# Kernel tuning notes

Hardware: AMD Instinct MI355X
Metric: run time of the kernel (lower is better)

Reference implementation:

```python
import jax, jax.numpy as jnp
import numpy as np

B, N, D = 16, 1000, 256
K_MAX = 512  # static upper bound on union size (k1 + k2 < K_MAX)


def setup_inputs() -> dict:
    key = jax.random.key(0)
    ks = jax.random.split(key, 6)
    a = jax.random.uniform(ks[0], (B, N, N), jnp.float32)
    a = a + jnp.swapaxes(a, 1, 2)  # symmetric
    adj = (a > 1.8).astype(jnp.float32)  # sparse-ish symmetric adjacency
    H1 = jax.random.normal(ks[1], (B, N, D), jnp.float32)
    H2 = jax.random.normal(ks[2], (B, N, D), jnp.float32)
    # per-batch permutations of node ids: row j of H_i corresponds to node idx_i[b, j]
    idx1 = jax.vmap(lambda k: jax.random.permutation(k, N))(jax.random.split(ks[3], B)).astype(jnp.int32)
    idx2 = jax.vmap(lambda k: jax.random.permutation(k, N))(jax.random.split(ks[4], B)).astype(jnp.int32)
    k1 = jax.random.randint(ks[5], (B,), 1, K_MAX // 2, jnp.int32)
    k2 = jax.random.randint(jax.random.fold_in(key, 7), (B,), 1, K_MAX // 2, jnp.int32)
    return {"adj": adj, "H1": H1, "H2": H2, "idx1": idx1, "idx2": idx2, "k1": k1, "k2": k2}


def _pool_one(adj_b, H1_b, H2_b, i1, i2, kk1, kk2):
    # adj_b: [N,N], H1_b/H2_b: [N,D], i1/i2: [N] node-id permutations, kk1/kk2: scalar keep counts
    pos = jnp.arange(N)
    # membership masks over node ids: node i1[j] selected iff j < kk1
    m1 = jnp.zeros((N,), bool).at[i1].set(pos < kk1)
    m2 = jnp.zeros((N,), bool).at[i2].set(pos < kk2)
    union = m1 | m2
    inter = m1 & m2
    # inverse permutations: position of node v within index list i1/i2
    inv1 = jnp.zeros((N,), jnp.int32).at[i1].set(pos.astype(jnp.int32))
    inv2 = jnp.zeros((N,), jnp.int32).at[i2].set(pos.astype(jnp.int32))
    H1n = H1_b[inv1]  # [N,D] features re-indexed by node id
    H2n = H2_b[inv2]
    # merged per-node feature: average on intersection, single-branch otherwise
    h = jnp.where(inter[:, None], 0.5 * (H1n + H2n),
                  jnp.where(m1[:, None], H1n,
                            jnp.where(m2[:, None], H2n, jnp.zeros_like(H1n))))
    # stable sort: union nodes first (ascending node id), then the rest; take K_MAX slots
    order = jnp.argsort(jnp.logical_not(union))[:K_MAX]
    valid = union[order]  # contiguous prefix of True
    new_mask = valid.astype(adj_b.dtype)  # [K_MAX]
    S = adj_b[order] * new_mask[:, None]  # [K_MAX, N] selected adjacency rows
    new_H = h[order] * new_mask[:, None]  # [K_MAX, D]
    new_adj = S @ adj_b @ S.T  # [K_MAX, K_MAX]
    return new_H, new_adj, new_mask


def reference(adj, H1, H2, idx1, idx2, k1, k2):
    return jax.vmap(_pool_one)(adj, H1, H2, idx1, idx2, k1, k2)
```

## Files before the change

### kernel.cpp

```cpp
#include <hip/hip_runtime.h>

#define BATCH 16
#define NN 1000
#define DD 256
#define KMAX 512

#define META_STRIDE 2560
#define AP 1024

typedef unsigned char u8;
typedef __attribute__((ext_vector_type(4))) int i32x4;

#define LD4(p) (*(const float4*)(p))

__device__ __forceinline__ void meta_body(
    int b, int t,
    const int* __restrict__ idx1, const int* __restrict__ idx2,
    const int* __restrict__ k1, const int* __restrict__ k2,
    int* __restrict__ meta) {
  __shared__ int sc[256];
  __shared__ int sU;
  int* inv1 = meta + (size_t)b * META_STRIDE;
  int* inv2 = inv1 + NN;
  int* order = inv2 + NN;
  int* Uptr = order + KMAX;
  const int* i1 = idx1 + (size_t)b * NN;
  const int* i2 = idx2 + (size_t)b * NN;
  for (int j = t; j < NN; j += 256) {
    inv1[i1[j]] = j;
    inv2[i2[j]] = j;
  }
  __syncthreads();
  int kk1 = k1[b], kk2 = k2[b];
  int base = t * 4;
  int un[4];
  int cnt = 0;
  for (int i = 0; i < 4; ++i) {
    int v = base + i;
    int u = 0;
    if (v < NN) u = (inv1[v] < kk1) || (inv2[v] < kk2);
    un[i] = u;
    cnt += u;
  }
  sc[t] = cnt;
  __syncthreads();
  for (int off = 1; off < 256; off <<= 1) {
    int v = (t >= off) ? sc[t - off] : 0;
    __syncthreads();
    sc[t] += v;
    __syncthreads();
  }
  int pref = sc[t] - cnt;
  for (int i = 0; i < 4; ++i)
    if (un[i]) order[pref++] = base + i;
  if (t == 255) {
    sU = sc[255];
    *Uptr = sc[255];
  }
  __syncthreads();
  int U = sU;
  for (int r = U + t; r < KMAX; r += 256) order[r] = 0;
}

__global__ __launch_bounds__(256) void meta_kernel(
    const int* __restrict__ idx1, const int* __restrict__ idx2,
    const int* __restrict__ k1, const int* __restrict__ k2,
    int* __restrict__ meta) {
  meta_body(blockIdx.x, threadIdx.x, idx1, idx2, k1, k2, meta);
}

__device__ __forceinline__ unsigned int pack4u8(float4 f) {
  return (unsigned int)(u8)f.x | ((unsigned int)(u8)f.y << 8) |
         ((unsigned int)(u8)f.z << 16) | ((unsigned int)(u8)f.w << 24);
}

__global__ __launch_bounds__(256) void convmeta_kernel(
    const float* __restrict__ adj, u8* __restrict__ adjb,
    const int* __restrict__ idx1, const int* __restrict__ idx2,
    const int* __restrict__ k1, const int* __restrict__ k2,
    int* __restrict__ meta) {
  int g = blockIdx.x;
  int tid = threadIdx.x;
  if (g >= 4096) {
    meta_body(g - 4096, tid, idx1, idx2, k1, k2, meta);
    return;
  }
  int xcd = g & 7, slot = g >> 3;
  int b = xcd + 8 * (slot >> 8);
  int r = (slot & 255) * 4 + (tid >> 6);
  int lane = tid & 63;
  int c0 = lane * 16;
  unsigned int w0 = 0, w1 = 0, w2 = 0, w3 = 0;
  if (r < NN) {
    const float* src = adj + ((size_t)b * NN + r) * NN + c0;
    int nv = NN - c0;
    if (nv >= 16) {
      w0 = pack4u8(LD4(src));
      w1 = pack4u8(LD4(src + 4));
      w2 = pack4u8(LD4(src + 8));
      w3 = pack4u8(LD4(src + 12));
    } else if (nv >= 8) {
      w0 = pack4u8(LD4(src));
      w1 = pack4u8(LD4(src + 4));
    }
  }
  *(int4*)(adjb + ((size_t)b * AP + r) * AP + c0) = make_int4(w0, w1, w2, w3);
}

__global__ __launch_bounds__(256) void conv_fb_kernel(
    const float* __restrict__ adj, u8* __restrict__ adjb, int bbase) {
  int bz = blockIdx.y;
  int b = bbase + bz;
  int tid = threadIdx.x;
  int r = blockIdx.x * 4 + (tid >> 6);
  int lane = tid & 63;
  int c0 = lane * 16;
  unsigned int w0 = 0, w1 = 0, w2 = 0, w3 = 0;
  if (r < NN) {
    const float* src = adj + ((size_t)b * NN + r) * NN + c0;
    int nv = NN - c0;
    if (nv >= 16) {
      w0 = pack4u8(LD4(src));
      w1 = pack4u8(LD4(src + 4));
      w2 = pack4u8(LD4(src + 8));
      w3 = pack4u8(LD4(src + 12));
    } else if (nv >= 8) {
      w0 = pack4u8(LD4(src));
      w1 = pack4u8(LD4(src + 4));
    }
  }
  *(int4*)(adjb + ((size_t)bz * AP + r) * AP + c0) = make_int4(w0, w1, w2, w3);
}

__device__ __forceinline__ void feat_row(
    const float* __restrict__ H1, const float* __restrict__ H2,
    const int* __restrict__ k1, const int* __restrict__ k2,
    const int* __restrict__ meta, float* __restrict__ outH,
    float* __restrict__ outMask, int b, int r, int l) {
  const int* inv1 = meta + (size_t)b * META_STRIDE;
  const int* inv2 = inv1 + NN;
  const int* order = inv2 + NN;
  int U = order[KMAX];
  float4* oH = (float4*)(outH + ((size_t)b * KMAX + r) * DD) + l;
  if (r >= U) {
    *oH = make_float4(0.f, 0.f, 0.f, 0.f);
    if (l == 0) outMask[(size_t)b * KMAX + r] = 0.f;
    return;
  }
  int v = order[r];
  int j1 = inv1[v];
  int j2 = inv2[v];
  bool in1 = j1 < k1[b];
  bool in2 = j2 < k2[b];
  const float4* h1 = (const float4*)(H1 + ((size_t)b * NN + j1) * DD) + l;
  const float4* h2 = (const float4*)(H2 + ((size_t)b * NN + j2) * DD) + l;
  float4 o;
  if (in1 && in2) {
    float4 a = *h1, c = *h2;
    o = make_float4(0.5f * (a.x + c.x), 0.5f * (a.y + c.y),
                    0.5f * (a.z + c.z), 0.5f * (a.w + c.w));
  } else if (in1) {
    o = *h1;
  } else {
    o = *h2;
  }
  *oH = o;
  if (l == 0) outMask[(size_t)b * KMAX + r] = 1.f;
}

__global__ __launch_bounds__(256) void feat_kernel(
    const float* __restrict__ H1, const float* __restrict__ H2,
    const int* __restrict__ k1, const int* __restrict__ k2,
    const int* __restrict__ meta,
    float* __restrict__ outH, float* __restrict__ outMask, int bbase) {
  int tid = threadIdx.x;
  int r = blockIdx.x * 4 + (tid >> 6);
  int b = blockIdx.y + bbase;
  feat_row(H1, H2, k1, k2, meta, outH, outMask, b, r, tid & 63);
}

template<int WHICH, int BM, int BN, bool PIN, bool FEAT>
__global__ __launch_bounds__(256) void mm_kernel(
    const u8* __restrict__ adjb, u8* __restrict__ Tb,
    const int* __restrict__ meta, float* __restrict__ outAdj,
    const float* __restrict__ H1, const float* __restrict__ H2,
    const int* __restrict__ k1, const int* __restrict__ k2,
    float* __restrict__ outH, float* __restrict__ outMask, int bbase) {
  constexpr int MR = BM / 32;
  constexpr int NR = BN / 32;
  constexpr int LA = (BM * 128) / 4096;
  constexpr int LB = (BN * 128) / 4096;
  constexpr int LL = LA + LB;
  constexpr int CT_TILES = (WHICH == 1 ? AP : KMAX) / BN;
  constexpr int RT_TILES = KMAX / BM;
  constexpr int TILES = RT_TILES * CT_TILES;
  constexpr int MMBLK = 8 * 2 * TILES;
  constexpr int NKT = AP / 128;

  int tid = threadIdx.x;

  if (FEAT && PIN && (int)blockIdx.x >= MMBLK) {
    int g2 = blockIdx.x - MMBLK;
    int xcd = g2 & 7;
    int slot = g2 >> 3;
    int b = xcd + 8 * (slot >> 6);
    int rb = slot & 63;
    int l = tid & 63;
#pragma unroll
    for (int pass = 0; pass < 2; ++pass) {
      int r = rb * 8 + pass * 4 + (tid >> 6);
      feat_row(H1, H2, k1, k2, meta, outH, outMask, b, r, l);
    }
    return;
  }

  int bz, rt, ct;
  if (PIN) {
    int g = blockIdx.x;
    int xcd = g & 7;
    int slot = g >> 3;
    bz = xcd + 8 * (slot / TILES);
    int tt = slot % TILES;
    rt = tt / CT_TILES;
    ct = tt % CT_TILES;
  } else {
    bz = blockIdx.z;
    rt = blockIdx.y;
    ct = blockIdx.x;
  }
  int b = PIN ? bz : (bz + bbase);

  const int* order = meta + (size_t)b * META_STRIDE + 2 * NN;
  int U = order[KMAX];
  int lane = tid & 63;
  int w = tid >> 6;
  int wr = w >> 1, wc = w & 1;

  __shared__ __align__(16) u8 A0[BM * 128];
  __shared__ __align__(16) u8 B0[BN * 128];
  __shared__ __align__(16) u8 A1[BM * 128];
  __shared__ __align__(16) u8 B1[BN * 128];
  __shared__ int sOrd[64];

  const u8* adjbB = adjb + (size_t)bz * AP * AP;
  const u8* TbB = Tb + (size_t)bz * KMAX * AP;

  bool active;
  if (WHICH == 1) {
    active = (rt * BM < U);
    if (!active) return;
  } else {
    active = (rt * BM < U) && (ct * BN < U);
  }

  if (tid < 64) sOrd[tid] = order[((WHICH == 1) ? rt * BM : ct * BN) + tid];
  __syncthreads();

  i32x4 acc[MR][NR] = {};

#define WAITV(N) asm volatile("s_waitcnt vmcnt(%0)" :: "i"(N) : "memory")
#define BARx() do { asm volatile("" ::: "memory"); __builtin_amdgcn_s_barrier(); \
                    asm volatile("" ::: "memory"); } while (0)

#define STAGE(ABUF, BBUF, KT)                                                  \
  {                                                                            \
    int k0 = (KT) * 128;                                                       \
    _Pragma("unroll")                                                          \
    for (int i = 0; i < LA; ++i) {                                             \
      int p = i * 256 + tid;                                                   \
      int r = p >> 3, cp = p & 7;                                              \
      int cs = cp ^ (r & 7);                                                   \
      const u8* src = (WHICH == 1)                                             \
          ? adjbB + (size_t)sOrd[r] * AP + k0 + cs * 16                        \
          : TbB + (size_t)(rt * BM + r) * AP + k0 + cs * 16;                   \
      u8* dst = (ABUF) + (size_t)(i * 256 + (tid & 192)) * 16;                 \
      __builtin_amdgcn_global_load_lds(                                        \
          (const __attribute__((address_space(1))) void*)src,                  \
          (__attribute__((address_space(3))) void*)dst, 16, 0, 0);             \
    }                                                                          \
    _Pragma("unroll")                                                          \
    for (int i = 0; i < LB; ++i) {                                             \
      int p = i * 256 + tid;                                                   \
      int r = p >> 3, cp = p & 7;                                              \
      int cs = cp ^ (r & 7);                                                   \
      const u8* src = (WHICH == 1)                                             \
          ? adjbB + (size_t)(ct * BN + r) * AP + k0 + cs * 16                  \
          : adjbB + (size_t)sOrd[r] * AP + k0 + cs * 16;                       \
      u8* dst = (BBUF) + (size_t)(i * 256 + (tid & 192)) * 16;                 \
      __builtin_amdgcn_global_load_lds(                                        \
          (const __attribute__((address_space(1))) void*)src,                  \
          (__attribute__((address_space(3))) void*)dst, 16, 0, 0);             \
    }                                                                          \
  }

#define COMPUTE128(ABUF, BBUF)                                                 \
  {                                                                            \
    _Pragma("unroll")                                                          \
    for (int s = 0; s < 2; ++s) {                                              \
      i32x4 a[MR], bv[NR];                                                     \
      _Pragma("unroll")                                                        \
      for (int m = 0; m < MR; ++m) {                                           \
        int row = wr * (MR * 16) + m * 16 + (lane & 15);                       \
        int c = (s * 4 + (lane >> 4)) ^ (row & 7);                             \
        a[m] = *(const i32x4*)((ABUF) + row * 128 + c * 16);                   \
      }                                                                        \
      _Pragma("unroll")                                                        \
      for (int n = 0; n < NR; ++n) {                                           \
        int row = wc * (NR * 16) + n * 16 + (lane & 15);                       \
        int c = (s * 4 + (lane >> 4)) ^ (row & 7);                             \
        bv[n] = *(const i32x4*)((BBUF) + row * 128 + c * 16);                  \
      }                                                                        \
      __builtin_amdgcn_s_setprio(1);                                           \
      _Pragma("unroll")                                                        \
      for (int m = 0; m < MR; ++m)                                             \
        _Pragma("unroll")                                                      \
        for (int n = 0; n < NR; ++n)                                           \
          acc[m][n] = __builtin_amdgcn_mfma_i32_16x16x64_i8(a[m], bv[n],       \
                                                            acc[m][n], 0, 0, 0); \
      __builtin_amdgcn_s_setprio(0);                                           \
    }                                                                          \
  }

  if (active) {
    STAGE(A0, B0, 0);
    STAGE(A1, B1, 1);
#pragma unroll 1
    for (int t = 0; t < NKT - 2; t += 2) {
      WAITV(LL);
      BARx();
      COMPUTE128(A0, B0);
      BARx();
      STAGE(A0, B0, t + 2);
      WAITV(LL);
      BARx();
      COMPUTE128(A1, B1);
      BARx();
      STAGE(A1, B1, t + 3);
    }
    WAITV(LL);
    BARx();
    COMPUTE128(A0, B0);
    WAITV(0);
    BARx();
    COMPUTE128(A1, B1);
  }
#undef STAGE
#undef COMPUTE128
#undef WAITV
#undef BARx

  if (WHICH == 1) {
    u8* TbW = Tb + (size_t)bz * KMAX * AP;
#pragma unroll
    for (int m = 0; m < MR; ++m)
#pragma unroll
      for (int n = 0; n < NR; ++n)
#pragma unroll
        for (int i = 0; i < 4; ++i) {
          int row = rt * BM + wr * (MR * 16) + m * 16 + ((lane >> 4) << 2) + i;
          int col = ct * BN + wc * (NR * 16) + n * 16 + (lane & 15);
          TbW[(size_t)row * AP + col] = (u8)acc[m][n][i];
        }
  } else {
    float* O = outAdj + (size_t)b * KMAX * KMAX;
#pragma unroll
    for (int m = 0; m < MR; ++m)
#pragma unroll
      for (int n = 0; n < NR; ++n)
#pragma unroll
        for (int i = 0; i < 4; ++i) {
          int row = rt * BM + wr * (MR * 16) + m * 16 + ((lane >> 4) << 2) + i;
          int col = ct * BN + wc * (NR * 16) + n * 16 + (lane & 15);
          float v = (row < U && col < U) ? (float)acc[m][n][i] : 0.f;
          O[(size_t)row * KMAX + col] = v;
        }
  }
}

extern "C" void kernel_launch(void* const* d_in, const int* in_sizes, int n_in,
                              void* d_out, int out_size, void* d_ws, size_t ws_size,
                              hipStream_t stream) {
  const float* adj = (const float*)d_in[0];
  const float* H1 = (const float*)d_in[1];
  const float* H2 = (const float*)d_in[2];
  const int* idx1 = (const int*)d_in[3];
  const int* idx2 = (const int*)d_in[4];
  const int* k1 = (const int*)d_in[5];
  const int* k2 = (const int*)d_in[6];

  float* outH = (float*)d_out;
  float* outAdj = outH + (size_t)BATCH * KMAX * DD;
  float* outMask = outAdj + (size_t)BATCH * KMAX * KMAX;

  int* meta = (int*)d_ws;
  size_t meta_bytes = (size_t)BATCH * META_STRIDE * sizeof(int);
  size_t meta_al = (meta_bytes + 255) & ~(size_t)255;

  size_t adjb_one = (size_t)AP * AP;
  size_t T_one = (size_t)KMAX * AP;
  size_t per_b = adjb_one + T_one;

  int chunk = 1;
  if (ws_size > meta_al + per_b)
    chunk = (int)((ws_size - meta_al) / per_b);
  if (chunk > BATCH) chunk = BATCH;
  if (chunk < 1) chunk = 1;

  u8* adjb = (u8*)((char*)d_ws + meta_al);
  u8* Tb = adjb + (size_t)chunk * adjb_one;

  if (chunk == BATCH) {
    convmeta_kernel<<<dim3(4096 + 16), 256, 0, stream>>>(adj, adjb, idx1, idx2,
                                                         k1, k2, meta);
    mm_kernel<1, 64, 128, true, true><<<dim3(2048), 256, 0, stream>>>(
        adjb, Tb, meta, outAdj, H1, H2, k1, k2, outH, outMask, 0);
    mm_kernel<2, 64, 64, true, false><<<dim3(1024), 256, 0, stream>>>(
        adjb, Tb, meta, outAdj, H1, H2, k1, k2, outH, outMask, 0);
  } else {
    meta_kernel<<<dim3(BATCH), 256, 0, stream>>>(idx1, idx2, k1, k2, meta);
    feat_kernel<<<dim3(KMAX / 4, BATCH), 256, 0, stream>>>(H1, H2, k1, k2, meta,
                                                           outH, outMask, 0);
    for (int bb = 0; bb < BATCH; bb += chunk) {
      int nb = (BATCH - bb < chunk) ? (BATCH - bb) : chunk;
      conv_fb_kernel<<<dim3(256, nb), 256, 0, stream>>>(adj, adjb, bb);
      mm_kernel<1, 64, 128, false, false><<<dim3(8, 8, nb), 256, 0, stream>>>(
          adjb, Tb, meta, outAdj, H1, H2, k1, k2, outH, outMask, bb);
      mm_kernel<2, 64, 64, false, false><<<dim3(8, 8, nb), 256, 0, stream>>>(
          adjb, Tb, meta, outAdj, H1, H2, k1, k2, outH, outMask, bb);
    }
  }
}
```

Measured before the change: 39.79 us.

## Use 4-stage LDS pipeline with 64x64 tiles and coalesced u8 conversion

Replaces the double-buffered A/B LDS staging with a four-buffer ring that prefetches three k-tiles ahead and needs one barrier per step instead of two. The first GEMM is fixed to 64x64 tiles, so it launches more blocks (3072 grid) and gets more parallelism per batch. The fp32-to-u8 adjacency conversion now has each lane handle strided 4-element chunks, giving coalesced 4-byte stores instead of 16-byte per-lane chunks. Extra LDS use and smaller tiles may reduce occupancy or data reuse.

```diff
diff --git a/kernel.cpp b/kernel.cpp
--- a/kernel.cpp
+++ b/kernel.cpp
@@ -74,6 +74,20 @@
          ((unsigned int)(u8)f.z << 16) | ((unsigned int)(u8)f.w << 24);
 }
 
+__device__ __forceinline__ void conv_rows(
+    const float* __restrict__ adj, u8* __restrict__ adjb,
+    int b_src, int b_dst, int r, int l) {
+  const float* srcrow = adj + ((size_t)b_src * NN + r) * NN;
+  u8* dstrow = adjb + ((size_t)b_dst * AP + r) * AP;
+#pragma unroll
+  for (int j = 0; j < 4; ++j) {
+    int idx = l + 64 * j;
+    unsigned int w = 0;
+    if (r < NN && idx < 250) w = pack4u8(LD4(srcrow + idx * 4));
+    *(unsigned int*)(dstrow + idx * 4) = w;
+  }
+}
+
 __global__ __launch_bounds__(256) void convmeta_kernel(
     const float* __restrict__ adj, u8* __restrict__ adjb,
     const int* __restrict__ idx1, const int* __restrict__ idx2,
@@ -88,48 +102,15 @@
   int xcd = g & 7, slot = g >> 3;
   int b = xcd + 8 * (slot >> 8);
   int r = (slot & 255) * 4 + (tid >> 6);
-  int lane = tid & 63;
-  int c0 = lane * 16;
-  unsigned int w0 = 0, w1 = 0, w2 = 0, w3 = 0;
-  if (r < NN) {
-    const float* src = adj + ((size_t)b * NN + r) * NN + c0;
-    int nv = NN - c0;
-    if (nv >= 16) {
-      w0 = pack4u8(LD4(src));
-      w1 = pack4u8(LD4(src + 4));
-      w2 = pack4u8(LD4(src + 8));
-      w3 = pack4u8(LD4(src + 12));
-    } else if (nv >= 8) {
-      w0 = pack4u8(LD4(src));
-      w1 = pack4u8(LD4(src + 4));
-    }
-  }
-  *(int4*)(adjb + ((size_t)b * AP + r) * AP + c0) = make_int4(w0, w1, w2, w3);
+  conv_rows(adj, adjb, b, b, r, tid & 63);
 }
 
 __global__ __launch_bounds__(256) void conv_fb_kernel(
     const float* __restrict__ adj, u8* __restrict__ adjb, int bbase) {
   int bz = blockIdx.y;
-  int b = bbase + bz;
   int tid = threadIdx.x;
   int r = blockIdx.x * 4 + (tid >> 6);
-  int lane = tid & 63;
-  int c0 = lane * 16;
-  unsigned int w0 = 0, w1 = 0, w2 = 0, w3 = 0;
-  if (r < NN) {
-    const float* src = adj + ((size_t)b * NN + r) * NN + c0;
-    int nv = NN - c0;
-    if (nv >= 16) {
-      w0 = pack4u8(LD4(src));
-      w1 = pack4u8(LD4(src + 4));
-      w2 = pack4u8(LD4(src + 8));
-      w3 = pack4u8(LD4(src + 12));
-    } else if (nv >= 8) {
-      w0 = pack4u8(LD4(src));
-      w1 = pack4u8(LD4(src + 4));
-    }
-  }
-  *(int4*)(adjb + ((size_t)bz * AP + r) * AP + c0) = make_int4(w0, w1, w2, w3);
+  conv_rows(adj, adjb, bbase + bz, bz, r, tid & 63);
 }
 
 __device__ __forceinline__ void feat_row(
@@ -179,23 +160,20 @@
   feat_row(H1, H2, k1, k2, meta, outH, outMask, b, r, tid & 63);
 }
 
-template<int WHICH, int BM, int BN, bool PIN, bool FEAT>
+template<int WHICH, bool PIN, bool FEAT>
 __global__ __launch_bounds__(256) void mm_kernel(
     const u8* __restrict__ adjb, u8* __restrict__ Tb,
     const int* __restrict__ meta, float* __restrict__ outAdj,
     const float* __restrict__ H1, const float* __restrict__ H2,
     const int* __restrict__ k1, const int* __restrict__ k2,
     float* __restrict__ outH, float* __restrict__ outMask, int bbase) {
-  constexpr int MR = BM / 32;
-  constexpr int NR = BN / 32;
-  constexpr int LA = (BM * 128) / 4096;
-  constexpr int LB = (BN * 128) / 4096;
-  constexpr int LL = LA + LB;
+  constexpr int BM = 64, BN = 64;
+  constexpr int MR = 2, NR = 2;
+  constexpr int LA = 2, LB = 2;
   constexpr int CT_TILES = (WHICH == 1 ? AP : KMAX) / BN;
   constexpr int RT_TILES = KMAX / BM;
   constexpr int TILES = RT_TILES * CT_TILES;
   constexpr int MMBLK = 8 * 2 * TILES;
-  constexpr int NKT = AP / 128;
 
   int tid = threadIdx.x;
 
@@ -236,10 +214,8 @@
   int w = tid >> 6;
   int wr = w >> 1, wc = w & 1;
 
-  __shared__ __align__(16) u8 A0[BM * 128];
-  __shared__ __align__(16) u8 B0[BN * 128];
-  __shared__ __align__(16) u8 A1[BM * 128];
-  __shared__ __align__(16) u8 B1[BN * 128];
+  __shared__ __align__(16) u8 As[4][BM * 128];
+  __shared__ __align__(16) u8 Bs[4][BN * 128];
   __shared__ int sOrd[64];
 
   const u8* adjbB = adjb + (size_t)bz * AP * AP;
@@ -262,8 +238,10 @@
 #define BARx() do { asm volatile("" ::: "memory"); __builtin_amdgcn_s_barrier(); \
                     asm volatile("" ::: "memory"); } while (0)
 
-#define STAGE(ABUF, BBUF, KT)                                                  \
+#define STAGE(BI, KT)                                                          \
   {                                                                            \
+    u8* sa_ = &As[(BI)][0];                                                    \
+    u8* sb_ = &Bs[(BI)][0];                                                    \
     int k0 = (KT) * 128;                                                       \
     _Pragma("unroll")                                                          \
     for (int i = 0; i < LA; ++i) {                                             \
@@ -273,7 +251,7 @@
       const u8* src = (WHICH == 1)                                             \
           ? adjbB + (size_t)sOrd[r] * AP + k0 + cs * 16                        \
           : TbB + (size_t)(rt * BM + r) * AP + k0 + cs * 16;                   \
-      u8* dst = (ABUF) + (size_t)(i * 256 + (tid & 192)) * 16;                 \
+      u8* dst = sa_ + (size_t)(i * 256 + (tid & 192)) * 16;                    \
       __builtin_amdgcn_global_load_lds(                                        \
           (const __attribute__((address_space(1))) void*)src,                  \
           (__attribute__((address_space(3))) void*)dst, 16, 0, 0);             \
@@ -286,15 +264,17 @@
       const u8* src = (WHICH == 1)                                             \
           ? adjbB + (size_t)(ct * BN + r) * AP + k0 + cs * 16                  \
           : adjbB + (size_t)sOrd[r] * AP + k0 + cs * 16;                       \
-      u8* dst = (BBUF) + (size_t)(i * 256 + (tid & 192)) * 16;                 \
+      u8* dst = sb_ + (size_t)(i * 256 + (tid & 192)) * 16;                    \
       __builtin_amdgcn_global_load_lds(                                        \
           (const __attribute__((address_space(1))) void*)src,                  \
           (__attribute__((address_space(3))) void*)dst, 16, 0, 0);             \
     }                                                                          \
   }
 
-#define COMPUTE128(ABUF, BBUF)                                                 \
+#define COMPUTE128(BI)                                                         \
   {                                                                            \
+    const u8* ca_ = &As[(BI)][0];                                              \
+    const u8* cb_ = &Bs[(BI)][0];                                              \
     _Pragma("unroll")                                                          \
     for (int s = 0; s < 2; ++s) {                                              \
       i32x4 a[MR], bv[NR];                                                     \
@@ -302,13 +282,13 @@
       for (int m = 0; m < MR; ++m) {                                           \
         int row = wr * (MR * 16) + m * 16 + (lane & 15);                       \
         int c = (s * 4 + (lane >> 4)) ^ (row & 7);                             \
-        a[m] = *(const i32x4*)((ABUF) + row * 128 + c * 16);                   \
+        a[m] = *(const i32x4*)(ca_ + row * 128 + c * 16);                      \
       }                                                                        \
       _Pragma("unroll")                                                        \
       for (int n = 0; n < NR; ++n) {                                           \
         int row = wc * (NR * 16) + n * 16 + (lane & 15);                       \
         int c = (s * 4 + (lane >> 4)) ^ (row & 7);                             \
-        bv[n] = *(const i32x4*)((BBUF) + row * 128 + c * 16);                  \
+        bv[n] = *(const i32x4*)(cb_ + row * 128 + c * 16);                     \
       }                                                                        \
       __builtin_amdgcn_s_setprio(1);                                           \
       _Pragma("unroll")                                                        \
@@ -322,27 +302,19 @@
   }
 
   if (active) {
-    STAGE(A0, B0, 0);
-    STAGE(A1, B1, 1);
+    STAGE(0, 0);
+    STAGE(1, 1);
+    STAGE(2, 2);
 #pragma unroll 1
-    for (int t = 0; t < NKT - 2; t += 2) {
-      WAITV(LL);
+    for (int t = 0; t < 5; ++t) {
+      WAITV(8);
       BARx();
-      COMPUTE128(A0, B0);
-      BARx();
-      STAGE(A0, B0, t + 2);
-      WAITV(LL);
-      BARx();
-      COMPUTE128(A1, B1);
-      BARx();
-      STAGE(A1, B1, t + 3);
+      COMPUTE128(t & 3);
+      STAGE((t + 3) & 3, t + 3);
     }
-    WAITV(LL);
-    BARx();
-    COMPUTE128(A0, B0);
-    WAITV(0);
-    BARx();
-    COMPUTE128(A1, B1);
+    WAITV(8); BARx(); COMPUTE128(1);
+    WAITV(4); BARx(); COMPUTE128(2);
+    WAITV(0); BARx(); COMPUTE128(3);
   }
 #undef STAGE
 #undef COMPUTE128
@@ -412,9 +384,9 @@
   if (chunk == BATCH) {
     convmeta_kernel<<<dim3(4096 + 16), 256, 0, stream>>>(adj, adjb, idx1, idx2,
                                                          k1, k2, meta);
-    mm_kernel<1, 64, 128, true, true><<<dim3(2048), 256, 0, stream>>>(
+    mm_kernel<1, true, true><<<dim3(3072), 256, 0, stream>>>(
         adjb, Tb, meta, outAdj, H1, H2, k1, k2, outH, outMask, 0);
-    mm_kernel<2, 64, 64, true, false><<<dim3(1024), 256, 0, stream>>>(
+    mm_kernel<2, true, false><<<dim3(1024), 256, 0, stream>>>(
         adjb, Tb, meta, outAdj, H1, H2, k1, k2, outH, outMask, 0);
   } else {
     meta_kernel<<<dim3(BATCH), 256, 0, stream>>>(idx1, idx2, k1, k2, meta);
@@ -423,9 +395,9 @@
     for (int bb = 0; bb < BATCH; bb += chunk) {
       int nb = (BATCH - bb < chunk) ? (BATCH - bb) : chunk;
       conv_fb_kernel<<<dim3(256, nb), 256, 0, stream>>>(adj, adjb, bb);
-      mm_kernel<1, 64, 128, false, false><<<dim3(8, 8, nb), 256, 0, stream>>>(
+      mm_kernel<1, false, false><<<dim3(16, 8, nb), 256, 0, stream>>>(
           adjb, Tb, meta, outAdj, H1, H2, k1, k2, outH, outMask, bb);
-      mm_kernel<2, 64, 64, false, false><<<dim3(8, 8, nb), 256, 0, stream>>>(
+      mm_kernel<2, false, false><<<dim3(8, 8, nb), 256, 0, stream>>>(
           adjb, Tb, meta, outAdj, H1, H2, k1, k2, outH, outMask, bb);
     }
   }
```

Measured after the change: 47.86 us. 1.2x slower.
